# Kernel optimization log

Measured on AMD Instinct MI355X. Metric: run time of the kernel, lower is better.

The kernel has to match this reference:

```python
import jax, jax.numpy as jnp
import numpy as np
import math

B, S, E, H, FF = 2, 2048, 768, 12, 3072
D = E // H
SCALING = 1.0
EPS = 1e-5


def layer_norm(x, g, b):
    mu = jnp.mean(x, axis=-1, keepdims=True)
    var = jnp.var(x, axis=-1, keepdims=True)
    return (x - mu) * jax.lax.rsqrt(var + EPS) * g + b


def setup_inputs() -> dict:
    key = jax.random.key(0)
    ks = jax.random.split(key, 16)
    s_e = 1.0 / math.sqrt(E)
    s_f = 1.0 / math.sqrt(FF)
    inp = {
        "x": jax.random.normal(ks[0], (B, S, E), dtype=jnp.float32),
        "Wq": jax.random.uniform(ks[1], (E, E), jnp.float32, -s_e, s_e),
        "bq": jnp.zeros((E,), jnp.float32),
        "Wk": jax.random.uniform(ks[2], (E, E), jnp.float32, -s_e, s_e),
        "bk": jnp.zeros((E,), jnp.float32),
        "Wv": jax.random.uniform(ks[3], (E, E), jnp.float32, -s_e, s_e),
        "bv": jnp.zeros((E,), jnp.float32),
        "Wo": jax.random.uniform(ks[4], (E, E), jnp.float32, -s_e, s_e),
        "bo": jnp.zeros((E,), jnp.float32),
        "W1": jax.random.uniform(ks[5], (E, FF), jnp.float32, -s_e, s_e),
        "b1": jnp.zeros((FF,), jnp.float32),
        "W2": jax.random.uniform(ks[6], (FF, E), jnp.float32, -s_f, s_f),
        "b2": jnp.zeros((E,), jnp.float32),
        "g1": jnp.ones((E,), jnp.float32),
        "be1": jnp.zeros((E,), jnp.float32),
        "g2": jnp.ones((E,), jnp.float32),
        "be2": jnp.zeros((E,), jnp.float32),
    }
    return inp


def reference(x, Wq, bq, Wk, bk, Wv, bv, Wo, bo, W1, b1, W2, b2, g1, be1, g2, be2):
    # --- multi-head attention with ALiBi-style symmetric distance bias ---
    q = (x @ Wq + bq).reshape(B, S, H, D)
    k = (x @ Wk + bk).reshape(B, S, H, D)
    v = (x @ Wv + bv).reshape(B, S, H, D)
    scores = jnp.einsum("bqhd,bkhd->bhqk", q, k) / math.sqrt(D)
    pos = jnp.arange(S)
    alibi = -SCALING * jnp.abs(pos[None, :] - pos[:, None]).astype(jnp.float32)  # [S,S]
    scores = scores + alibi  # broadcast over [B,H]
    attn_map = jax.nn.softmax(scores, axis=-1)  # [B,H,S,S]
    ctx = jnp.einsum("bhqk,bkhd->bqhd", attn_map, v).reshape(B, S, E)
    attn_out = ctx @ Wo + bo
    # --- residual + norm, FFN, residual + norm (dropout = eval/identity) ---
    h = layer_norm(x + attn_out, g1, be1)
    ff = jax.nn.relu(h @ W1 + b1) @ W2 + b2
    out = layer_norm(h + ff, g2, be2)
    return (out, attn_map)
```

## Files before the change

### kernel.cpp

```cpp
#include <hip/hip_runtime.h>
#include <stdint.h>

static constexpr int cB = 2, cS = 2048, cE = 768, cH = 12, cFF = 3072, cD = 64;
static constexpr int cM = cB * cS;

typedef __bf16 bf16x8 __attribute__((ext_vector_type(8)));
typedef float f32x4 __attribute__((ext_vector_type(4)));

__device__ __forceinline__ unsigned short f2bf(float f) {
    union { float f; unsigned int u; } v; v.f = f;
    unsigned int r = v.u + 0x7fffu + ((v.u >> 16) & 1u);
    return (unsigned short)(r >> 16);
}

__device__ __forceinline__ void load_lds16(const unsigned short* g, unsigned short* l) {
    __builtin_amdgcn_global_load_lds(
        (const __attribute__((address_space(1))) unsigned int*)(g),
        (__attribute__((address_space(3))) unsigned int*)(l), 16, 0, 0);
}

template<int BM, int BN, int EPI>
__global__ __launch_bounds__(256) void gemm_nt(
    const unsigned short* __restrict__ Ab,
    const unsigned short* __restrict__ Btp,
    float* __restrict__ outF,
    unsigned short* __restrict__ outB,
    const float* __restrict__ bias0,
    const float* __restrict__ bias1,
    const float* __restrict__ bias2,
    const float* __restrict__ resid,
    int M, int N, int K, long sB)
{
    constexpr int MI = BM / 32, NI = BN / 32;
    __shared__ alignas(16) unsigned short Al[BM * 64];
    __shared__ alignas(16) unsigned short Bl[BN * 64];
    const int tid = threadIdx.x;
    const int lane = tid & 63, wave = tid >> 6;
    const int wm = wave >> 1, wn = wave & 1;
    const int bz = blockIdx.z;
    const int m0 = blockIdx.y * BM, n0 = blockIdx.x * BN;
    const int ln = lane & 15, lg = lane >> 4;
    const int sw = ln & 7;

    const unsigned short* Bt = Btp + (size_t)bz * sB;

    f32x4 acc[MI][NI];
#pragma unroll
    for (int i = 0; i < MI; i++)
#pragma unroll
        for (int j = 0; j < NI; j++) acc[i][j] = (f32x4){0.f, 0.f, 0.f, 0.f};

    for (int k0 = 0; k0 < K; k0 += 64) {
        __syncthreads();
#pragma unroll
        for (int it = 0; it < BM / 32; ++it) {
            int idx = tid + it * 256;
            int r = idx >> 3, c8 = idx & 7;
            int cs = c8 ^ (r & 7);
            load_lds16(Ab + (size_t)(m0 + r) * K + k0 + cs * 8, &Al[idx * 8]);
        }
#pragma unroll
        for (int it = 0; it < BN / 32; ++it) {
            int idx = tid + it * 256;
            int r = idx >> 3, c8 = idx & 7;
            int cs = c8 ^ (r & 7);
            load_lds16(Bt + (size_t)(n0 + r) * K + k0 + cs * 8, &Bl[idx * 8]);
        }
        __syncthreads();
#pragma unroll
        for (int ks = 0; ks < 2; ++ks) {
            bf16x8 av[MI], bv[NI];
#pragma unroll
            for (int i = 0; i < MI; i++) {
                int row = wm * (BM / 2) + 16 * i + ln;
                av[i] = *(const bf16x8*)&Al[row * 64 + ((ks * 4 + lg) ^ sw) * 8];
            }
#pragma unroll
            for (int j = 0; j < NI; j++) {
                int row = wn * (BN / 2) + 16 * j + ln;
                bv[j] = *(const bf16x8*)&Bl[row * 64 + ((ks * 4 + lg) ^ sw) * 8];
            }
#pragma unroll
            for (int i = 0; i < MI; i++)
#pragma unroll
                for (int j = 0; j < NI; j++)
                    acc[i][j] = __builtin_amdgcn_mfma_f32_16x16x32_bf16(av[i], bv[j], acc[i][j], 0, 0, 0);
        }
    }

#pragma unroll
    for (int i = 0; i < MI; i++) {
#pragma unroll
        for (int j = 0; j < NI; j++) {
#pragma unroll
            for (int r = 0; r < 4; r++) {
                int m = m0 + wm * (BM / 2) + 16 * i + lg * 4 + r;
                int n = n0 + wn * (BN / 2) + 16 * j + ln;
                float v = acc[i][j][r];
                if constexpr (EPI == 0) {
                    const float* bia = (bz == 0) ? bias0 : ((bz == 1) ? bias1 : bias2);
                    v += bia[n];
                    int b = m >> 11, s = m & 2047, h = n >> 6, d = n & 63;
                    outB[(size_t)bz * ((size_t)cB * cH * cS * cD) +
                         ((((size_t)b * cH + h) * cS + s) << 6) + d] = f2bf(v);
                } else if constexpr (EPI == 3) {
                    v += bias0[n] + resid[(size_t)m * N + n];
                    outF[(size_t)m * N + n] = v;
                } else {
                    v = fmaxf(v + bias0[n], 0.f);
                    outB[(size_t)m * N + n] = f2bf(v);
                }
            }
        }
    }
}

__global__ __launch_bounds__(256, 3) void attn_fused(
    const unsigned short* __restrict__ Qh,
    const unsigned short* __restrict__ Kh,
    const unsigned short* __restrict__ Vt,
    float* __restrict__ attn,
    unsigned short* __restrict__ ctxb)
{
    constexpr int VS = 136;
    __shared__ alignas(16) unsigned short Ql[64 * 64];
    __shared__ alignas(16) unsigned short KVl[128 * 64];
    __shared__ alignas(16) unsigned short Pb[64 * VS];
    __shared__ float rs2[2][64];
    __shared__ float rsinv[64];

    const int tid = threadIdx.x;
    const int lane = tid & 63, wave = tid >> 6;
    const int wm = wave >> 1, wn = wave & 1;
    const int ln = lane & 15, lg = lane >> 4;
    const int sw = ln & 7;
    const int m0 = blockIdx.x * 64;
    const int bh = blockIdx.y;

    const unsigned short* Qg = Qh + ((size_t)bh * cS + m0) * cD;
    const unsigned short* Kg = Kh + (size_t)bh * cS * cD;
    const unsigned short* Vg = Vt + (size_t)bh * cD * cS;
    float* attng = attn + (size_t)bh * cS * cS;

#pragma unroll
    for (int it = 0; it < 2; ++it) {
        int idx = tid + it * 256;
        int r = idx >> 3, c8 = idx & 7;
        int cs = c8 ^ (r & 7);
        load_lds16(Qg + r * cD + cs * 8, &Ql[idx * 8]);
    }

    float psum[8];
#pragma unroll
    for (int k = 0; k < 8; k++) psum[k] = 0.f;

    for (int nt = 0; nt < 16; ++nt) {
        __syncthreads();
#pragma unroll
        for (int it = 0; it < 4; ++it) {
            int idx = tid + it * 256;
            int r = idx >> 3, c8 = idx & 7;
            int cs = c8 ^ (r & 7);
            load_lds16(Kg + (size_t)(nt * 128 + r) * cD + cs * 8, &KVl[idx * 8]);
        }
        __syncthreads();
        f32x4 acc[2][4];
#pragma unroll
        for (int i = 0; i < 2; i++)
#pragma unroll
            for (int j = 0; j < 4; j++) acc[i][j] = (f32x4){0.f, 0.f, 0.f, 0.f};
#pragma unroll
        for (int ks = 0; ks < 2; ++ks) {
            bf16x8 a[2], b[4];
#pragma unroll
            for (int i = 0; i < 2; i++)
                a[i] = *(const bf16x8*)&Ql[(wm * 32 + 16 * i + ln) * 64 + ((ks * 4 + lg) ^ sw) * 8];
#pragma unroll
            for (int j = 0; j < 4; j++)
                b[j] = *(const bf16x8*)&KVl[(wn * 64 + 16 * j + ln) * 64 + ((ks * 4 + lg) ^ sw) * 8];
#pragma unroll
            for (int i = 0; i < 2; i++)
#pragma unroll
                for (int j = 0; j < 4; j++)
                    acc[i][j] = __builtin_amdgcn_mfma_f32_16x16x32_bf16(a[i], b[j], acc[i][j], 0, 0, 0);
        }
#pragma unroll
        for (int i = 0; i < 2; i++)
#pragma unroll
            for (int j = 0; j < 4; j++)
#pragma unroll
                for (int r = 0; r < 4; r++) {
                    int mg = m0 + wm * 32 + 16 * i + lg * 4 + r;
                    int ng = nt * 128 + wn * 64 + 16 * j + ln;
                    psum[i * 4 + r] += __expf(acc[i][j][r] * 0.125f - fabsf((float)(mg - ng)));
                }
    }
#pragma unroll
    for (int k = 0; k < 8; k++) {
        float v = psum[k];
        v += __shfl_xor(v, 1); v += __shfl_xor(v, 2);
        v += __shfl_xor(v, 4); v += __shfl_xor(v, 8);
        psum[k] = v;
    }
    if (ln == 0) {
#pragma unroll
        for (int i = 0; i < 2; i++)
#pragma unroll
            for (int r = 0; r < 4; r++)
                rs2[wn][wm * 32 + 16 * i + lg * 4 + r] = psum[i * 4 + r];
    }
    __syncthreads();
    if (tid < 64) rsinv[tid] = 1.f / (rs2[0][tid] + rs2[1][tid]);
    __syncthreads();
    float invl[8];
#pragma unroll
    for (int i = 0; i < 2; i++)
#pragma unroll
        for (int r = 0; r < 4; r++)
            invl[i * 4 + r] = rsinv[wm * 32 + 16 * i + lg * 4 + r];

    f32x4 oacc[2][2];
#pragma unroll
    for (int i = 0; i < 2; i++)
#pragma unroll
        for (int j = 0; j < 2; j++) oacc[i][j] = (f32x4){0.f, 0.f, 0.f, 0.f};

    for (int nt = 0; nt < 16; ++nt) {
        __syncthreads();
#pragma unroll
        for (int it = 0; it < 4; ++it) {
            int idx = tid + it * 256;
            int r = idx >> 3, c8 = idx & 7;
            int cs = c8 ^ (r & 7);
            load_lds16(Kg + (size_t)(nt * 128 + r) * cD + cs * 8, &KVl[idx * 8]);
        }
        __syncthreads();
        f32x4 acc[2][4];
#pragma unroll
        for (int i = 0; i < 2; i++)
#pragma unroll
            for (int j = 0; j < 4; j++) acc[i][j] = (f32x4){0.f, 0.f, 0.f, 0.f};
#pragma unroll
        for (int ks = 0; ks < 2; ++ks) {
            bf16x8 a[2], b[4];
#pragma unroll
            for (int i = 0; i < 2; i++)
                a[i] = *(const bf16x8*)&Ql[(wm * 32 + 16 * i + ln) * 64 + ((ks * 4 + lg) ^ sw) * 8];
#pragma unroll
            for (int j = 0; j < 4; j++)
                b[j] = *(const bf16x8*)&KVl[(wn * 64 + 16 * j + ln) * 64 + ((ks * 4 + lg) ^ sw) * 8];
#pragma unroll
            for (int i = 0; i < 2; i++)
#pragma unroll
                for (int j = 0; j < 4; j++)
                    acc[i][j] = __builtin_amdgcn_mfma_f32_16x16x32_bf16(a[i], b[j], acc[i][j], 0, 0, 0);
        }
#pragma unroll
        for (int i = 0; i < 2; i++)
#pragma unroll
            for (int j = 0; j < 4; j++)
#pragma unroll
                for (int r = 0; r < 4; r++) {
                    int mloc = wm * 32 + 16 * i + lg * 4 + r;
                    int nloc = wn * 64 + 16 * j + ln;
                    int mg = m0 + mloc, ng = nt * 128 + nloc;
                    float p = __expf(acc[i][j][r] * 0.125f - fabsf((float)(mg - ng))) * invl[i * 4 + r];
                    attng[(size_t)mg * cS + ng] = p;
                    Pb[mloc * VS + nloc] = f2bf(p);
                }
        __syncthreads();
#pragma unroll
        for (int it = 0; it < 4; ++it) {
            int idx = tid + it * 256;
            int r = idx >> 4, c8 = idx & 15;
            int cs = c8 ^ (r & 7);
            load_lds16(Vg + (size_t)r * cS + nt * 128 + cs * 8, &KVl[idx * 8]);
        }
        __syncthreads();
#pragma unroll
        for (int ks = 0; ks < 4; ++ks) {
            bf16x8 pa[2], vb[2];
#pragma unroll
            for (int i = 0; i < 2; i++)
                pa[i] = *(const bf16x8*)&Pb[(wm * 32 + 16 * i + ln) * VS + ks * 32 + lg * 8];
#pragma unroll
            for (int j = 0; j < 2; j++) {
                int row = wn * 32 + 16 * j + ln;
                vb[j] = *(const bf16x8*)&KVl[row * 128 + ((ks * 4 + lg) ^ sw) * 8];
            }
#pragma unroll
            for (int i = 0; i < 2; i++)
#pragma unroll
                for (int j = 0; j < 2; j++)
                    oacc[i][j] = __builtin_amdgcn_mfma_f32_16x16x32_bf16(pa[i], vb[j], oacc[i][j], 0, 0, 0);
        }
    }
    {
        int b = bh / cH, h = bh % cH;
#pragma unroll
        for (int i = 0; i < 2; i++)
#pragma unroll
            for (int j = 0; j < 2; j++)
#pragma unroll
                for (int r = 0; r < 4; r++) {
                    int mg = m0 + wm * 32 + 16 * i + lg * 4 + r;
                    int d = wn * 32 + 16 * j + ln;
                    ctxb[((size_t)b * cS + mg) * cE + h * 64 + d] = f2bf(oacc[i][j][r]);
                }
    }
}

template<bool WH>
__global__ __launch_bounds__(256) void layernorm_k(const float* __restrict__ in,
    const float* __restrict__ g, const float* __restrict__ be,
    float* __restrict__ outF, unsigned short* __restrict__ outB)
{
    const size_t row = blockIdx.x;
    const float* p = in + row * cE;
    const int tid = threadIdx.x;
    float x0 = p[tid], x1 = p[tid + 256], x2 = p[tid + 512];
    float sum = x0 + x1 + x2, sq = x0 * x0 + x1 * x1 + x2 * x2;
    __shared__ float s1[4], s2[4];
    for (int o = 32; o; o >>= 1) { sum += __shfl_xor(sum, o); sq += __shfl_xor(sq, o); }
    if ((tid & 63) == 0) { s1[tid >> 6] = sum; s2[tid >> 6] = sq; }
    __syncthreads();
    sum = s1[0] + s1[1] + s1[2] + s1[3];
    sq  = s2[0] + s2[1] + s2[2] + s2[3];
    float mu = sum * (1.f / cE);
    float var = sq * (1.f / cE) - mu * mu;
    float rstd = rsqrtf(var + 1e-5f);
#pragma unroll
    for (int i = 0; i < 3; i++) {
        int c = tid + 256 * i;
        float xv = (i == 0) ? x0 : ((i == 1) ? x1 : x2);
        float y = (xv - mu) * rstd * g[c] + be[c];
        outF[row * cE + c] = y;
        if constexpr (WH) outB[row * cE + c] = f2bf(y);
    }
}

__global__ __launch_bounds__(256) void transpose_f32_bf16(const float* __restrict__ src,
    unsigned short* __restrict__ dst, int R, int C)
{
    __shared__ float t[32][33];
    int c0 = blockIdx.x * 32, r0 = blockIdx.y * 32;
    int tx = threadIdx.x & 31, ty = threadIdx.x >> 5;
#pragma unroll
    for (int i = 0; i < 32; i += 8) t[ty + i][tx] = src[(size_t)(r0 + ty + i) * C + c0 + tx];
    __syncthreads();
#pragma unroll
    for (int i = 0; i < 32; i += 8) dst[(size_t)(c0 + ty + i) * R + r0 + tx] = f2bf(t[tx][ty + i]);
}

__global__ __launch_bounds__(256) void transpose_bf16_b(const unsigned short* __restrict__ src,
    unsigned short* __restrict__ dst, int R, int C)
{
    __shared__ unsigned short t[32][33];
    int c0 = blockIdx.x * 32, r0 = blockIdx.y * 32;
    size_t zo = (size_t)blockIdx.z * R * C;
    int tx = threadIdx.x & 31, ty = threadIdx.x >> 5;
#pragma unroll
    for (int i = 0; i < 32; i += 8) t[ty + i][tx] = src[zo + (size_t)(r0 + ty + i) * C + c0 + tx];
    __syncthreads();
#pragma unroll
    for (int i = 0; i < 32; i += 8) dst[zo + (size_t)(c0 + ty + i) * R + r0 + tx] = t[tx][ty + i];
}

__global__ __launch_bounds__(256) void f32_to_bf16_k(const float* __restrict__ src,
    unsigned short* __restrict__ dst)
{
    int i = blockIdx.x * 256 + threadIdx.x;
    float4 v = ((const float4*)src)[i];
    ushort4 o;
    o.x = f2bf(v.x); o.y = f2bf(v.y); o.z = f2bf(v.z); o.w = f2bf(v.w);
    ((ushort4*)dst)[i] = o;
}

extern "C" void kernel_launch(void* const* d_in, const int* in_sizes, int n_in,
                              void* d_out, int out_size, void* d_ws, size_t ws_size,
                              hipStream_t stream)
{
    const float* x   = (const float*)d_in[0];
    const float* Wq  = (const float*)d_in[1];
    const float* bq  = (const float*)d_in[2];
    const float* Wk  = (const float*)d_in[3];
    const float* bk  = (const float*)d_in[4];
    const float* Wv  = (const float*)d_in[5];
    const float* bv  = (const float*)d_in[6];
    const float* Wo  = (const float*)d_in[7];
    const float* bo  = (const float*)d_in[8];
    const float* W1  = (const float*)d_in[9];
    const float* b1  = (const float*)d_in[10];
    const float* W2  = (const float*)d_in[11];
    const float* b2  = (const float*)d_in[12];
    const float* g1  = (const float*)d_in[13];
    const float* be1 = (const float*)d_in[14];
    const float* g2  = (const float*)d_in[15];
    const float* be2 = (const float*)d_in[16];

    float* out  = (float*)d_out;
    float* attn = out + (size_t)cB * cS * cE;

    char* ws = (char*)d_ws;
    unsigned short* xb   = (unsigned short*)(ws + 0);
    unsigned short* ctxb = xb;
    unsigned short* Wqt  = (unsigned short*)(ws + 6291456);
    unsigned short* W1t  = (unsigned short*)(ws + 11010048);
    unsigned short* W2t  = (unsigned short*)(ws + 15728640);
    unsigned short* Qh   = (unsigned short*)(ws + 20447232);
    unsigned short* Kh   = (unsigned short*)(ws + 26738688);
    unsigned short* Vh   = (unsigned short*)(ws + 33030144);
    unsigned short* Vt   = (unsigned short*)(ws + 39321600);
    unsigned short* ff1b = Qh;
    float* res1 = (float*)(ws + 45613056);
    float* res2 = res1;
    float* hf   = (float*)(ws + 58195968);
    unsigned short* hb = (unsigned short*)(ws + 70778880);

    f32_to_bf16_k<<<(cM * cE) / 1024, 256, 0, stream>>>(x, xb);
    transpose_f32_bf16<<<dim3(24, 24), 256, 0, stream>>>(Wq, Wqt, cE, cE);
    transpose_f32_bf16<<<dim3(24, 24), 256, 0, stream>>>(Wk, Wqt + 589824, cE, cE);
    transpose_f32_bf16<<<dim3(24, 24), 256, 0, stream>>>(Wv, Wqt + 2 * 589824, cE, cE);
    transpose_f32_bf16<<<dim3(24, 24), 256, 0, stream>>>(Wo, Wqt + 3 * 589824, cE, cE);
    transpose_f32_bf16<<<dim3(96, 24), 256, 0, stream>>>(W1, W1t, cE, cFF);
    transpose_f32_bf16<<<dim3(24, 96), 256, 0, stream>>>(W2, W2t, cFF, cE);
    gemm_nt<128, 128, 0><<<dim3(6, 32, 3), 256, 0, stream>>>(
        xb, Wqt, nullptr, Qh, bq, bk, bv, nullptr, cM, cE, cE, 589824);
    transpose_bf16_b<<<dim3(2, 64, cB * cH), 256, 0, stream>>>(Vh, Vt, cS, cD);
    attn_fused<<<dim3(cS / 64, cB * cH), 256, 0, stream>>>(Qh, Kh, Vt, attn, ctxb);
    gemm_nt<64, 128, 3><<<dim3(6, 64, 1), 256, 0, stream>>>(
        ctxb, Wqt + 3 * 589824, res1, nullptr, bo, nullptr, nullptr, x, cM, cE, cE, 0);
    layernorm_k<true><<<cM, 256, 0, stream>>>(res1, g1, be1, hf, hb);
    gemm_nt<128, 128, 4><<<dim3(24, 32, 1), 256, 0, stream>>>(
        hb, W1t, nullptr, ff1b, b1, nullptr, nullptr, nullptr, cM, cFF, cE, 0);
    gemm_nt<64, 128, 3><<<dim3(6, 64, 1), 256, 0, stream>>>(
        ff1b, W2t, res2, nullptr, b2, nullptr, nullptr, hf, cM, cE, cFF, 0);
    layernorm_k<false><<<cM, 256, 0, stream>>>(res2, g2, be2, out, nullptr);
}
```

Before: 692.9 us.

## Fuse prep kernels, keep Q in registers, prefetch V with K, retile output GEMMs

```diff
diff --git a/kernel.cpp b/kernel.cpp
--- a/kernel.cpp
+++ b/kernel.cpp
@@ -123,8 +123,8 @@
     unsigned short* __restrict__ ctxb)
 {
     constexpr int VS = 136;
-    __shared__ alignas(16) unsigned short Ql[64 * 64];
-    __shared__ alignas(16) unsigned short KVl[128 * 64];
+    __shared__ alignas(16) unsigned short Kl[128 * 64];
+    __shared__ alignas(16) unsigned short Vl[64 * 128];
     __shared__ alignas(16) unsigned short Pb[64 * VS];
     __shared__ float rs2[2][64];
     __shared__ float rsinv[64];
@@ -147,8 +147,15 @@
         int idx = tid + it * 256;
         int r = idx >> 3, c8 = idx & 7;
         int cs = c8 ^ (r & 7);
-        load_lds16(Qg + r * cD + cs * 8, &Ql[idx * 8]);
-    }
+        load_lds16(Qg + r * cD + cs * 8, &Vl[idx * 8]);
+    }
+    __syncthreads();
+    bf16x8 qf[2][2];
+#pragma unroll
+    for (int ks = 0; ks < 2; ++ks)
+#pragma unroll
+        for (int i = 0; i < 2; i++)
+            qf[ks][i] = *(const bf16x8*)&Vl[(wm * 32 + 16 * i + ln) * 64 + ((ks * 4 + lg) ^ sw) * 8];
 
     float psum[8];
 #pragma unroll
@@ -161,7 +168,7 @@
             int idx = tid + it * 256;
             int r = idx >> 3, c8 = idx & 7;
             int cs = c8 ^ (r & 7);
-            load_lds16(Kg + (size_t)(nt * 128 + r) * cD + cs * 8, &KVl[idx * 8]);
+            load_lds16(Kg + (size_t)(nt * 128 + r) * cD + cs * 8, &Kl[idx * 8]);
         }
         __syncthreads();
         f32x4 acc[2][4];
@@ -171,18 +178,15 @@
             for (int j = 0; j < 4; j++) acc[i][j] = (f32x4){0.f, 0.f, 0.f, 0.f};
 #pragma unroll
         for (int ks = 0; ks < 2; ++ks) {
-            bf16x8 a[2], b[4];
+            bf16x8 b[4];
+#pragma unroll
+            for (int j = 0; j < 4; j++)
+                b[j] = *(const bf16x8*)&Kl[(wn * 64 + 16 * j + ln) * 64 + ((ks * 4 + lg) ^ sw) * 8];
 #pragma unroll
             for (int i = 0; i < 2; i++)
-                a[i] = *(const bf16x8*)&Ql[(wm * 32 + 16 * i + ln) * 64 + ((ks * 4 + lg) ^ sw) * 8];
-#pragma unroll
-            for (int j = 0; j < 4; j++)
-                b[j] = *(const bf16x8*)&KVl[(wn * 64 + 16 * j + ln) * 64 + ((ks * 4 + lg) ^ sw) * 8];
-#pragma unroll
-            for (int i = 0; i < 2; i++)
 #pragma unroll
                 for (int j = 0; j < 4; j++)
-                    acc[i][j] = __builtin_amdgcn_mfma_f32_16x16x32_bf16(a[i], b[j], acc[i][j], 0, 0, 0);
+                    acc[i][j] = __builtin_amdgcn_mfma_f32_16x16x32_bf16(qf[ks][i], b[j], acc[i][j], 0, 0, 0);
         }
 #pragma unroll
         for (int i = 0; i < 2; i++)
@@ -232,7 +236,14 @@
             int idx = tid + it * 256;
             int r = idx >> 3, c8 = idx & 7;
             int cs = c8 ^ (r & 7);
-            load_lds16(Kg + (size_t)(nt * 128 + r) * cD + cs * 8, &KVl[idx * 8]);
+            load_lds16(Kg + (size_t)(nt * 128 + r) * cD + cs * 8, &Kl[idx * 8]);
+        }
+#pragma unroll
+        for (int it = 0; it < 4; ++it) {
+            int idx = tid + it * 256;
+            int r = idx >> 4, c8 = idx & 15;
+            int cs = c8 ^ (r & 7);
+            load_lds16(Vg + (size_t)r * cS + nt * 128 + cs * 8, &Vl[idx * 8]);
         }
         __syncthreads();
         f32x4 acc[2][4];
@@ -242,18 +253,15 @@
             for (int j = 0; j < 4; j++) acc[i][j] = (f32x4){0.f, 0.f, 0.f, 0.f};
 #pragma unroll
         for (int ks = 0; ks < 2; ++ks) {
-            bf16x8 a[2], b[4];
+            bf16x8 b[4];
+#pragma unroll
+            for (int j = 0; j < 4; j++)
+                b[j] = *(const bf16x8*)&Kl[(wn * 64 + 16 * j + ln) * 64 + ((ks * 4 + lg) ^ sw) * 8];
 #pragma unroll
             for (int i = 0; i < 2; i++)
-                a[i] = *(const bf16x8*)&Ql[(wm * 32 + 16 * i + ln) * 64 + ((ks * 4 + lg) ^ sw) * 8];
-#pragma unroll
-            for (int j = 0; j < 4; j++)
-                b[j] = *(const bf16x8*)&KVl[(wn * 64 + 16 * j + ln) * 64 + ((ks * 4 + lg) ^ sw) * 8];
-#pragma unroll
-            for (int i = 0; i < 2; i++)
 #pragma unroll
                 for (int j = 0; j < 4; j++)
-                    acc[i][j] = __builtin_amdgcn_mfma_f32_16x16x32_bf16(a[i], b[j], acc[i][j], 0, 0, 0);
+                    acc[i][j] = __builtin_amdgcn_mfma_f32_16x16x32_bf16(qf[ks][i], b[j], acc[i][j], 0, 0, 0);
         }
 #pragma unroll
         for (int i = 0; i < 2; i++)
@@ -270,14 +278,6 @@
                 }
         __syncthreads();
 #pragma unroll
-        for (int it = 0; it < 4; ++it) {
-            int idx = tid + it * 256;
-            int r = idx >> 4, c8 = idx & 15;
-            int cs = c8 ^ (r & 7);
-            load_lds16(Vg + (size_t)r * cS + nt * 128 + cs * 8, &KVl[idx * 8]);
-        }
-        __syncthreads();
-#pragma unroll
         for (int ks = 0; ks < 4; ++ks) {
             bf16x8 pa[2], vb[2];
 #pragma unroll
@@ -286,7 +286,7 @@
 #pragma unroll
             for (int j = 0; j < 2; j++) {
                 int row = wn * 32 + 16 * j + ln;
-                vb[j] = *(const bf16x8*)&KVl[row * 128 + ((ks * 4 + lg) ^ sw) * 8];
+                vb[j] = *(const bf16x8*)&Vl[row * 128 + ((ks * 4 + lg) ^ sw) * 8];
             }
 #pragma unroll
             for (int i = 0; i < 2; i++)
@@ -339,17 +339,45 @@
     }
 }
 
-__global__ __launch_bounds__(256) void transpose_f32_bf16(const float* __restrict__ src,
-    unsigned short* __restrict__ dst, int R, int C)
+__global__ __launch_bounds__(256) void prep_all(
+    const float* __restrict__ x, unsigned short* __restrict__ xb,
+    const float* __restrict__ Wq, const float* __restrict__ Wk,
+    const float* __restrict__ Wv, const float* __restrict__ Wo,
+    const float* __restrict__ W1, const float* __restrict__ W2,
+    unsigned short* __restrict__ Wqt, unsigned short* __restrict__ W1t,
+    unsigned short* __restrict__ W2t)
 {
     __shared__ float t[32][33];
-    int c0 = blockIdx.x * 32, r0 = blockIdx.y * 32;
-    int tx = threadIdx.x & 31, ty = threadIdx.x >> 5;
-#pragma unroll
-    for (int i = 0; i < 32; i += 8) t[ty + i][tx] = src[(size_t)(r0 + ty + i) * C + c0 + tx];
-    __syncthreads();
-#pragma unroll
-    for (int i = 0; i < 32; i += 8) dst[(size_t)(c0 + ty + i) * R + r0 + tx] = f2bf(t[tx][ty + i]);
+    int bid = blockIdx.x;
+    if (bid < 3072) {
+        int i = bid * 256 + threadIdx.x;
+        float4 v = ((const float4*)x)[i];
+        ushort4 o;
+        o.x = f2bf(v.x); o.y = f2bf(v.y); o.z = f2bf(v.z); o.w = f2bf(v.w);
+        ((ushort4*)xb)[i] = o;
+        return;
+    }
+    bid -= 3072;
+    const float* src; unsigned short* dst; int R, C, tx, ty;
+    if (bid < 2304) {
+        int m = bid / 576, tt = bid - m * 576;
+        src = (m == 0) ? Wq : (m == 1) ? Wk : (m == 2) ? Wv : Wo;
+        dst = Wqt + (size_t)m * 589824;
+        R = 768; C = 768; tx = tt % 24; ty = tt / 24;
+    } else if (bid < 4608) {
+        int tt = bid - 2304;
+        src = W1; dst = W1t; R = 768; C = 3072; tx = tt % 96; ty = tt / 96;
+    } else {
+        int tt = bid - 4608;
+        src = W2; dst = W2t; R = 3072; C = 768; tx = tt % 24; ty = tt / 24;
+    }
+    int c0 = tx * 32, r0 = ty * 32;
+    int lx = threadIdx.x & 31, ly = threadIdx.x >> 5;
+#pragma unroll
+    for (int i = 0; i < 32; i += 8) t[ly + i][lx] = src[(size_t)(r0 + ly + i) * C + c0 + lx];
+    __syncthreads();
+#pragma unroll
+    for (int i = 0; i < 32; i += 8) dst[(size_t)(c0 + ly + i) * R + r0 + lx] = f2bf(t[lx][ly + i]);
 }
 
 __global__ __launch_bounds__(256) void transpose_bf16_b(const unsigned short* __restrict__ src,
@@ -364,16 +392,6 @@
     __syncthreads();
 #pragma unroll
     for (int i = 0; i < 32; i += 8) dst[zo + (size_t)(c0 + ty + i) * R + r0 + tx] = t[tx][ty + i];
-}
-
-__global__ __launch_bounds__(256) void f32_to_bf16_k(const float* __restrict__ src,
-    unsigned short* __restrict__ dst)
-{
-    int i = blockIdx.x * 256 + threadIdx.x;
-    float4 v = ((const float4*)src)[i];
-    ushort4 o;
-    o.x = f2bf(v.x); o.y = f2bf(v.y); o.z = f2bf(v.z); o.w = f2bf(v.w);
-    ((ushort4*)dst)[i] = o;
 }
 
 extern "C" void kernel_launch(void* const* d_in, const int* in_sizes, int n_in,
@@ -417,23 +435,17 @@
     float* hf   = (float*)(ws + 58195968);
     unsigned short* hb = (unsigned short*)(ws + 70778880);
 
-    f32_to_bf16_k<<<(cM * cE) / 1024, 256, 0, stream>>>(x, xb);
-    transpose_f32_bf16<<<dim3(24, 24), 256, 0, stream>>>(Wq, Wqt, cE, cE);
-    transpose_f32_bf16<<<dim3(24, 24), 256, 0, stream>>>(Wk, Wqt + 589824, cE, cE);
-    transpose_f32_bf16<<<dim3(24, 24), 256, 0, stream>>>(Wv, Wqt + 2 * 589824, cE, cE);
-    transpose_f32_bf16<<<dim3(24, 24), 256, 0, stream>>>(Wo, Wqt + 3 * 589824, cE, cE);
-    transpose_f32_bf16<<<dim3(96, 24), 256, 0, stream>>>(W1, W1t, cE, cFF);
-    transpose_f32_bf16<<<dim3(24, 96), 256, 0, stream>>>(W2, W2t, cFF, cE);
+    prep_all<<<9984, 256, 0, stream>>>(x, xb, Wq, Wk, Wv, Wo, W1, W2, Wqt, W1t, W2t);
     gemm_nt<128, 128, 0><<<dim3(6, 32, 3), 256, 0, stream>>>(
         xb, Wqt, nullptr, Qh, bq, bk, bv, nullptr, cM, cE, cE, 589824);
     transpose_bf16_b<<<dim3(2, 64, cB * cH), 256, 0, stream>>>(Vh, Vt, cS, cD);
     attn_fused<<<dim3(cS / 64, cB * cH), 256, 0, stream>>>(Qh, Kh, Vt, attn, ctxb);
-    gemm_nt<64, 128, 3><<<dim3(6, 64, 1), 256, 0, stream>>>(
+    gemm_nt<64, 64, 3><<<dim3(12, 64, 1), 256, 0, stream>>>(
         ctxb, Wqt + 3 * 589824, res1, nullptr, bo, nullptr, nullptr, x, cM, cE, cE, 0);
     layernorm_k<true><<<cM, 256, 0, stream>>>(res1, g1, be1, hf, hb);
     gemm_nt<128, 128, 4><<<dim3(24, 32, 1), 256, 0, stream>>>(
         hb, W1t, nullptr, ff1b, b1, nullptr, nullptr, nullptr, cM, cFF, cE, 0);
-    gemm_nt<64, 128, 3><<<dim3(6, 64, 1), 256, 0, stream>>>(
+    gemm_nt<64, 64, 3><<<dim3(12, 64, 1), 256, 0, stream>>>(
         ff1b, W2t, res2, nullptr, b2, nullptr, nullptr, hf, cM, cE, cFF, 0);
     layernorm_k<false><<<cM, 256, 0, stream>>>(res2, g2, be2, out, nullptr);
 }
```

Result: faster. 663.9 us (-4.2%).
